# Performance work log

Hardware: AMD Instinct MI355X
Metric: run time of the kernel (lower is better)

Reference implementation:

```python
import jax, jax.numpy as jnp
import numpy as np

B, T, D = 2, 2048, 1024
H, G, K = 16, 4, 64          # num_heads, num_kv_heads, head_dim
R = H // G                   # GQA repeat factor
F = 4096                     # mlp_dim
EPS = 1e-6


def rms_norm(x, scale, eps=EPS):
    var = jnp.mean(x.astype(jnp.float32) ** 2, axis=-1, keepdims=True)
    normed = x * jax.lax.rsqrt(var + eps)
    return (scale * normed).astype(x.dtype)


def apply_rope(x_BTHK, sin_BTK, cos_BTK):
    half = x_BTHK.shape[-1] // 2
    x1, x2 = x_BTHK[..., :half], x_BTHK[..., half:]
    s = sin_BTK[:, :, None, :]
    c = cos_BTK[:, :, None, :]
    return jnp.concatenate([x1 * c - x2 * s, x2 * c + x1 * s], axis=-1).astype(x_BTHK.dtype)


def setup_inputs() -> dict:
    key = jax.random.key(0)
    ks = jax.random.split(key, 12)
    hidden_BTD = jax.random.normal(ks[0], (B, T, D), jnp.float32)
    # rope tables: realistic sin/cos of position*inv_freq
    inv_freq = 1.0 / (10000.0 ** (jnp.arange(K // 2, dtype=jnp.float32) / (K // 2)))
    ang = jnp.arange(T, dtype=jnp.float32)[:, None] * inv_freq[None, :]  # [T, K/2]
    sin_BTK = jnp.broadcast_to(jnp.sin(ang)[None], (B, T, K // 2))
    cos_BTK = jnp.broadcast_to(jnp.cos(ang)[None], (B, T, K // 2))
    mask = jnp.broadcast_to(jnp.tril(jnp.ones((T, T), bool))[None], (B, T, T))
    sc = 1.0 / np.sqrt(D)
    scf = 1.0 / np.sqrt(F)
    return {
        "hidden_BTD": hidden_BTD, "sin_BTK": sin_BTK, "cos_BTK": cos_BTK, "mask": mask,
        "ln1_scale": jnp.ones((D,), jnp.float32),
        "ln2_scale": jnp.ones((D,), jnp.float32),
        "qn_scale": jnp.ones((K,), jnp.float32),
        "kn_scale": jnp.ones((K,), jnp.float32),
        "q_w": jax.random.normal(ks[1], (D, H * K), jnp.float32) * sc,
        "k_w": jax.random.normal(ks[2], (D, G * K), jnp.float32) * sc,
        "v_w": jax.random.normal(ks[3], (D, G * K), jnp.float32) * sc,
        "o_w": jax.random.normal(ks[4], (H * K, D), jnp.float32) * sc,
        "gate_w": jax.random.normal(ks[5], (D, F), jnp.float32) * sc,
        "up_w": jax.random.normal(ks[6], (D, F), jnp.float32) * sc,
        "down_w": jax.random.normal(ks[7], (F, D), jnp.float32) * scf,
    }


def reference(hidden_BTD, sin_BTK, cos_BTK, mask, ln1_scale, ln2_scale,
              qn_scale, kn_scale, q_w, k_w, v_w, o_w, gate_w, up_w, down_w):
    x = rms_norm(hidden_BTD, ln1_scale)
    q = rms_norm((x @ q_w).reshape(B, T, H, K), qn_scale)
    k = rms_norm((x @ k_w).reshape(B, T, G, K), kn_scale)
    v = (x @ v_w).reshape(B, T, G, K)
    q = apply_rope(q, sin_BTK, cos_BTK)
    k = apply_rope(k, sin_BTK, cos_BTK)
    q_BTGRK = q.reshape(B, T, G, R, K)
    scale = K ** (-0.5)
    logits = jnp.einsum('BTGRK,BSGK->BTSGR', q_BTGRK, k) * scale
    neg = float(jnp.finfo(logits.dtype).min)
    logits = jnp.where(mask[:, :, :, None, None], logits, neg)
    weights = jax.nn.softmax(logits.astype(jnp.float32), axis=2).astype(logits.dtype)
    attn = jnp.einsum('BTSGR,BSGK->BTGRK', weights, v).reshape(B, T, H * K)
    hidden_BTD = hidden_BTD + attn @ o_w
    y = rms_norm(hidden_BTD, ln2_scale)
    ff = (jax.nn.silu(y @ gate_w) * (y @ up_w)) @ down_w
    return hidden_BTD + ff
```

## Files before the change

kernel.cpp:

```cpp
#include <hip/hip_runtime.h>
#include <hip/hip_bf16.h>

#define EPSF 1e-6f
constexpr int Bsz  = 2;
constexpr int Tseq = 2048;
constexpr int Dmod = 1024;
constexpr int Hh   = 16;
constexpr int Gg   = 4;
constexpr int Ff   = 4096;
constexpr int Mrows = Bsz * Tseq;

typedef __attribute__((ext_vector_type(8))) short bf16x8;
typedef __attribute__((ext_vector_type(4))) float f32x4;
typedef unsigned short u16;

__device__ inline u16 f2bf(float x) {
    union { float f; unsigned u; } v; v.f = x;
    unsigned r = v.u + 0x7fff + ((v.u >> 16) & 1);
    return (u16)(r >> 16);
}
__device__ inline float bf2f(u16 h) {
    union { unsigned u; float f; } v; v.u = ((unsigned)h) << 16; return v.f;
}

__device__ __forceinline__ void async_copy16(const u16* g, u16* l) {
    __builtin_amdgcn_global_load_lds(
        (const __attribute__((address_space(1))) void*)g,
        (__attribute__((address_space(3))) void*)l, 16, 0, 0);
}


__global__ __launch_bounds__(256) void wprep_all_kernel(
    const float* __restrict__ q_w, const float* __restrict__ k_w,
    const float* __restrict__ v_w, const float* __restrict__ o_w,
    const float* __restrict__ gate_w, const float* __restrict__ up_w,
    const float* __restrict__ down_w,
    u16* __restrict__ QKVT, u16* __restrict__ OTh, u16* __restrict__ OTl,
    u16* __restrict__ GTh, u16* __restrict__ UTh, u16* __restrict__ DTh)
{
    const int bx = blockIdx.x;
    const float* W; u16* Th; u16* Tl = nullptr;
    int N, Kd, ntile, ktile, drow;
    if (bx < 1024) {
        W = q_w; N = 1024; Kd = 1024; ntile = bx & 31; ktile = bx >> 5;
        Th = QKVT; drow = ntile * 32;
    } else if (bx < 1280) {
        const int i = bx - 1024;
        W = k_w; N = 256; Kd = 1024; ntile = i & 7; ktile = i >> 3;
        Th = QKVT; drow = 1024 + ntile * 32;
    } else if (bx < 1536) {
        const int i = bx - 1280;
        W = v_w; N = 256; Kd = 1024; ntile = i & 7; ktile = i >> 3;
        Th = QKVT; drow = 1280 + ntile * 32;
    } else if (bx < 2560) {
        const int i = bx - 1536;
        W = o_w; N = 1024; Kd = 1024; ntile = i & 31; ktile = i >> 5;
        Th = OTh; Tl = OTl; drow = ntile * 32;
    } else if (bx < 6656) {
        const int i = bx - 2560;
        W = gate_w; N = 4096; Kd = 1024; ntile = i & 127; ktile = i >> 7;
        Th = GTh; drow = ntile * 32;
    } else if (bx < 10752) {
        const int i = bx - 6656;
        W = up_w; N = 4096; Kd = 1024; ntile = i & 127; ktile = i >> 7;
        Th = UTh; drow = ntile * 32;
    } else {
        const int i = bx - 10752;
        W = down_w; N = 1024; Kd = 4096; ntile = i & 31; ktile = i >> 5;
        Th = DTh; drow = ntile * 32;
    }
    const int n0 = ntile * 32, k0 = ktile * 32;

    __shared__ float tile[32][33];
    const int r = threadIdx.x >> 3, c4 = (threadIdx.x & 7) * 4;
    const float4 v = *reinterpret_cast<const float4*>(&W[(size_t)(k0 + r) * N + n0 + c4]);
    tile[r][c4 + 0] = v.x; tile[r][c4 + 1] = v.y;
    tile[r][c4 + 2] = v.z; tile[r][c4 + 3] = v.w;
    __syncthreads();
    const int nl = threadIdx.x >> 3, kq = (threadIdx.x & 7) * 4;
    float x0 = tile[kq + 0][nl], x1 = tile[kq + 1][nl];
    float x2 = tile[kq + 2][nl], x3 = tile[kq + 3][nl];
    ushort4 h;
    h.x = f2bf(x0); h.y = f2bf(x1); h.z = f2bf(x2); h.w = f2bf(x3);
    *reinterpret_cast<ushort4*>(&Th[(size_t)(drow + nl) * Kd + k0 + kq]) = h;
    if (Tl) {
        ushort4 l;
        l.x = f2bf(x0 - bf2f(h.x)); l.y = f2bf(x1 - bf2f(h.y));
        l.z = f2bf(x2 - bf2f(h.z)); l.w = f2bf(x3 - bf2f(h.w));
        *reinterpret_cast<ushort4*>(&Tl[(size_t)(drow + nl) * Kd + k0 + kq]) = l;
    }
}

template <int LO>
__global__ __launch_bounds__(256) void rmsnorm_split_kernel(
    const float* __restrict__ x, const float* __restrict__ scale,
    u16* __restrict__ oh, u16* __restrict__ ol)
{
    const int row = blockIdx.x;
    const int tid = threadIdx.x;
    const float4 v = reinterpret_cast<const float4*>(x + (size_t)row * Dmod)[tid];
    float ss = v.x * v.x + v.y * v.y + v.z * v.z + v.w * v.w;
    #pragma unroll
    for (int off = 32; off; off >>= 1) ss += __shfl_xor(ss, off, 64);
    __shared__ float part[4];
    if ((tid & 63) == 0) part[tid >> 6] = ss;
    __syncthreads();
    const float tot = part[0] + part[1] + part[2] + part[3];
    const float rstd = rsqrtf(tot * (1.0f / Dmod) + EPSF);
    const float4 sc = reinterpret_cast<const float4*>(scale)[tid];
    float o0 = v.x * rstd * sc.x, o1 = v.y * rstd * sc.y;
    float o2 = v.z * rstd * sc.z, o3 = v.w * rstd * sc.w;
    ushort4 h;
    h.x = f2bf(o0); h.y = f2bf(o1); h.z = f2bf(o2); h.w = f2bf(o3);
    *reinterpret_cast<ushort4*>(&oh[(size_t)row * Dmod + tid * 4]) = h;
    if (LO) {
        ushort4 l;
        l.x = f2bf(o0 - bf2f(h.x)); l.y = f2bf(o1 - bf2f(h.y));
        l.z = f2bf(o2 - bf2f(h.z)); l.w = f2bf(o3 - bf2f(h.w));
        *reinterpret_cast<ushort4*>(&ol[(size_t)row * Dmod + tid * 4]) = l;
    }
}

template <int ASPLIT, int BSPLIT, int RES>
__global__ __launch_bounds__(256, 2) void mfma_gemm_kernel(
    const u16* __restrict__ Ah, const u16* __restrict__ Al,
    const u16* __restrict__ Bh, const u16* __restrict__ Bl,
    const float* __restrict__ res, float* __restrict__ C,
    int M, int N, int Kd)
{
    __shared__ u16 As_h[128 * 32];
    __shared__ u16 As_l[128 * 32];
    __shared__ u16 Bs_h[128 * 32];
    __shared__ u16 Bs_l[128 * 32];

    const int tid = threadIdx.x;
    const int lane = tid & 63, wave = tid >> 6;
    const int wm = (wave >> 1) * 64, wn = (wave & 1) * 64;
    const int m0 = blockIdx.y * 128, n0 = blockIdx.x * 128;
    const int fm = lane & 15, quad = lane >> 4;
    const int fsw = (fm >> 1) & 3;
    const int fcol = ((quad ^ fsw) * 8);

    f32x4 acc[4][4];
    #pragma unroll
    for (int i = 0; i < 4; ++i)
        #pragma unroll
        for (int j = 0; j < 4; ++j) acc[i][j] = (f32x4){0.f, 0.f, 0.f, 0.f};

    const int lrow = lane >> 2;
    const int lchunk = lane & 3;
    const int schunk = lchunk ^ ((lrow >> 1) & 3);

    for (int k0 = 0; k0 < Kd; k0 += 32) {
        __syncthreads();
        #pragma unroll
        for (int p = 0; p < 2; ++p) {
            const int row = wave * 32 + p * 16 + lrow;
            const size_t ga = (size_t)(m0 + row) * Kd + k0 + schunk * 8;
            const size_t gb = (size_t)(n0 + row) * Kd + k0 + schunk * 8;
            const int ls = row * 32 + lchunk * 8;
            async_copy16(&Ah[ga], &As_h[ls]);
            if (ASPLIT) async_copy16(&Al[ga], &As_l[ls]);
            async_copy16(&Bh[gb], &Bs_h[ls]);
            if (BSPLIT) async_copy16(&Bl[gb], &Bs_l[ls]);
        }
        __syncthreads();

        bf16x8 ah[4], al[4], bh[4], bl[4];
        #pragma unroll
        for (int t = 0; t < 4; ++t) {
            const int ra = (wm + t * 16 + fm) * 32 + fcol;
            const int rb = (wn + t * 16 + fm) * 32 + fcol;
            ah[t] = *reinterpret_cast<const bf16x8*>(&As_h[ra]);
            bh[t] = *reinterpret_cast<const bf16x8*>(&Bs_h[rb]);
            if (ASPLIT) al[t] = *reinterpret_cast<const bf16x8*>(&As_l[ra]);
            if (BSPLIT) bl[t] = *reinterpret_cast<const bf16x8*>(&Bs_l[rb]);
        }
        #pragma unroll
        for (int mt = 0; mt < 4; ++mt)
            #pragma unroll
            for (int nt = 0; nt < 4; ++nt) {
                acc[mt][nt] = __builtin_amdgcn_mfma_f32_16x16x32_bf16(
                    ah[mt], bh[nt], acc[mt][nt], 0, 0, 0);
                if (BSPLIT)
                    acc[mt][nt] = __builtin_amdgcn_mfma_f32_16x16x32_bf16(
                        ah[mt], bl[nt], acc[mt][nt], 0, 0, 0);
                if (ASPLIT)
                    acc[mt][nt] = __builtin_amdgcn_mfma_f32_16x16x32_bf16(
                        al[mt], bh[nt], acc[mt][nt], 0, 0, 0);
            }
    }

    const int cr = (lane >> 4) * 4, cn = lane & 15;
    #pragma unroll
    for (int mt = 0; mt < 4; ++mt)
        #pragma unroll
        for (int nt = 0; nt < 4; ++nt)
            #pragma unroll
            for (int r = 0; r < 4; ++r) {
                const int gm = m0 + wm + mt * 16 + cr + r;
                const int gn = n0 + wn + nt * 16 + cn;
                float v = acc[mt][nt][r];
                if (RES) v += res[(size_t)gm * N + gn];
                C[(size_t)gm * N + gn] = v;
            }
}

__global__ __launch_bounds__(256, 2) void qkv_fused_kernel(
    const u16* __restrict__ Ah, const u16* __restrict__ Bh,
    const float* __restrict__ qn, const float* __restrict__ kn,
    const float* __restrict__ sinp, const float* __restrict__ cosp,
    u16* __restrict__ Qbh, u16* __restrict__ Qbl,
    u16* __restrict__ Kbh, u16* __restrict__ Kbl,
    u16* __restrict__ Vth, u16* __restrict__ Vtl)
{
    __shared__ u16 As_h[128 * 32];
    __shared__ u16 Bs_h[128 * 32];

    const int Kd = 1024;
    const int tid = threadIdx.x;
    const int lane = tid & 63, wave = tid >> 6;
    const int wm = (wave >> 1) * 64, wn = (wave & 1) * 64;
    const int m0 = blockIdx.y * 128, n0 = blockIdx.x * 128;
    const int fm = lane & 15, quad = lane >> 4;
    const int fsw = (fm >> 1) & 3;
    const int fcol = ((quad ^ fsw) * 8);

    f32x4 acc[4][4];
    #pragma unroll
    for (int i = 0; i < 4; ++i)
        #pragma unroll
        for (int j = 0; j < 4; ++j) acc[i][j] = (f32x4){0.f, 0.f, 0.f, 0.f};

    const int lrow = lane >> 2;
    const int lchunk = lane & 3;
    const int schunk = lchunk ^ ((lrow >> 1) & 3);

    for (int k0 = 0; k0 < Kd; k0 += 32) {
        __syncthreads();
        #pragma unroll
        for (int p = 0; p < 2; ++p) {
            const int row = wave * 32 + p * 16 + lrow;
            const size_t ga = (size_t)(m0 + row) * Kd + k0 + schunk * 8;
            const size_t gb = (size_t)(n0 + row) * Kd + k0 + schunk * 8;
            const int ls = row * 32 + lchunk * 8;
            async_copy16(&Ah[ga], &As_h[ls]);
            async_copy16(&Bh[gb], &Bs_h[ls]);
        }
        __syncthreads();

        bf16x8 ah[4], bh[4];
        #pragma unroll
        for (int t = 0; t < 4; ++t) {
            ah[t] = *reinterpret_cast<const bf16x8*>(&As_h[(wm + t * 16 + fm) * 32 + fcol]);
            bh[t] = *reinterpret_cast<const bf16x8*>(&Bs_h[(wn + t * 16 + fm) * 32 + fcol]);
        }
        #pragma unroll
        for (int mt = 0; mt < 4; ++mt)
            #pragma unroll
            for (int nt = 0; nt < 4; ++nt)
                acc[mt][nt] = __builtin_amdgcn_mfma_f32_16x16x32_bf16(
                    ah[mt], bh[nt], acc[mt][nt], 0, 0, 0);
    }

    const int gn0 = n0 + wn;
    const int l15 = lane & 15;

    if (gn0 < 1280) {
        const bool isQ = (gn0 < 1024);
        const float* nsc = isQ ? qn : kn;
        const float osc = isQ ? 0.125f : 1.0f;
        u16* __restrict__ oh = isQ ? Qbh : Kbh;
        u16* __restrict__ ol = isQ ? Qbl : Kbl;
        const int rowstride = isQ ? 1024 : 256;
        const int colbase = isQ ? gn0 : gn0 - 1024;
        float sc[4];
        #pragma unroll
        for (int nt = 0; nt < 4; ++nt) sc[nt] = nsc[nt * 16 + l15];

        #pragma unroll
        for (int mt = 0; mt < 4; ++mt)
            #pragma unroll
            for (int r = 0; r < 4; ++r) {
                const int bt = m0 + wm + mt * 16 + quad * 4 + r;
                float v[4];
                #pragma unroll
                for (int nt = 0; nt < 4; ++nt) v[nt] = acc[mt][nt][r];
                float ss = v[0] * v[0] + v[1] * v[1] + v[2] * v[2] + v[3] * v[3];
                #pragma unroll
                for (int off = 1; off < 16; off <<= 1)
                    ss += __shfl_xor(ss, off, 16);
                const float rstd = rsqrtf(ss * (1.0f / 64.0f) + EPSF);
                float nv[4];
                #pragma unroll
                for (int nt = 0; nt < 4; ++nt) nv[nt] = v[nt] * rstd * sc[nt];
                const float s0 = sinp[bt * 32 + l15];
                const float c0 = cosp[bt * 32 + l15];
                const float s1 = sinp[bt * 32 + 16 + l15];
                const float c1 = cosp[bt * 32 + 16 + l15];
                float o[4];
                o[0] = (nv[0] * c0 - nv[2] * s0) * osc;
                o[1] = (nv[1] * c1 - nv[3] * s1) * osc;
                o[2] = (nv[2] * c0 + nv[0] * s0) * osc;
                o[3] = (nv[3] * c1 + nv[1] * s1) * osc;
                #pragma unroll
                for (int nt = 0; nt < 4; ++nt) {
                    const size_t off = (size_t)bt * rowstride + colbase + nt * 16 + l15;
                    const u16 hi = f2bf(o[nt]);
                    oh[off] = hi;
                    ol[off] = f2bf(o[nt] - bf2f(hi));
                }
            }
    } else {
        const int g = (gn0 - 1280) >> 6;
        const int b = (m0 + wm) >> 11;
        const int tb = ((m0 + wm) & 2047) + quad * 4;
        #pragma unroll
        for (int mt = 0; mt < 4; ++mt)
            #pragma unroll
            for (int nt = 0; nt < 4; ++nt) {
                const float v0 = acc[mt][nt][0], v1 = acc[mt][nt][1];
                const float v2 = acc[mt][nt][2], v3 = acc[mt][nt][3];
                ushort4 hv, lv;
                hv.x = f2bf(v0); hv.y = f2bf(v1); hv.z = f2bf(v2); hv.w = f2bf(v3);
                lv.x = f2bf(v0 - bf2f(hv.x)); lv.y = f2bf(v1 - bf2f(hv.y));
                lv.z = f2bf(v2 - bf2f(hv.z)); lv.w = f2bf(v3 - bf2f(hv.w));
                const size_t off =
                    ((size_t)((b * 4 + g) * 64 + nt * 16 + l15)) * Tseq + tb + mt * 16;
                *reinterpret_cast<ushort4*>(&Vth[off]) = hv;
                *reinterpret_cast<ushort4*>(&Vtl[off]) = lv;
            }
    }
}

__global__ __launch_bounds__(256, 2) void mfma_gateup_kernel(
    const u16* __restrict__ Ah, const u16* __restrict__ Al,
    const u16* __restrict__ Bg, const u16* __restrict__ Bu,
    u16* __restrict__ FF, int M, int N, int Kd)
{
    __shared__ u16 As_h[128 * 32];
    __shared__ u16 As_l[128 * 32];
    __shared__ u16 Gs[64 * 32];
    __shared__ u16 Us[64 * 32];

    const int tid = threadIdx.x;
    const int lane = tid & 63, wave = tid >> 6;
    const int wm = (wave >> 1) * 64, wn = (wave & 1) * 32;
    const int m0 = blockIdx.y * 128, n0 = blockIdx.x * 64;
    const int fm = lane & 15, quad = lane >> 4;
    const int fsw = (fm >> 1) & 3;
    const int fcol = ((quad ^ fsw) * 8);

    f32x4 accg[4][2], accu[4][2];
    #pragma unroll
    for (int i = 0; i < 4; ++i)
        #pragma unroll
        for (int j = 0; j < 2; ++j) {
            accg[i][j] = (f32x4){0.f, 0.f, 0.f, 0.f};
            accu[i][j] = (f32x4){0.f, 0.f, 0.f, 0.f};
        }

    const int lrow = lane >> 2;
    const int lchunk = lane & 3;
    const int schunk = lchunk ^ ((lrow >> 1) & 3);

    for (int k0 = 0; k0 < Kd; k0 += 32) {
        __syncthreads();
        #pragma unroll
        for (int p = 0; p < 2; ++p) {
            const int row = p * 64 + wave * 16 + lrow;
            const size_t ga = (size_t)(m0 + row) * Kd + k0 + schunk * 8;
            const int ls = row * 32 + lchunk * 8;
            async_copy16(&Ah[ga], &As_h[ls]);
            async_copy16(&Al[ga], &As_l[ls]);
        }
        {
            const int row = wave * 16 + lrow;
            const size_t gb = (size_t)(n0 + row) * Kd + k0 + schunk * 8;
            const int ls = row * 32 + lchunk * 8;
            async_copy16(&Bg[gb], &Gs[ls]);
            async_copy16(&Bu[gb], &Us[ls]);
        }
        __syncthreads();

        bf16x8 a_h[4], a_l[4], g_f[2], u_f[2];
        #pragma unroll
        for (int t = 0; t < 4; ++t) {
            const int ra = (wm + t * 16 + fm) * 32 + fcol;
            a_h[t] = *reinterpret_cast<const bf16x8*>(&As_h[ra]);
            a_l[t] = *reinterpret_cast<const bf16x8*>(&As_l[ra]);
        }
        #pragma unroll
        for (int j = 0; j < 2; ++j) {
            const int rb = (wn + j * 16 + fm) * 32 + fcol;
            g_f[j] = *reinterpret_cast<const bf16x8*>(&Gs[rb]);
            u_f[j] = *reinterpret_cast<const bf16x8*>(&Us[rb]);
        }
        #pragma unroll
        for (int mt = 0; mt < 4; ++mt)
            #pragma unroll
            for (int nt = 0; nt < 2; ++nt) {
                accg[mt][nt] = __builtin_amdgcn_mfma_f32_16x16x32_bf16(
                    a_h[mt], g_f[nt], accg[mt][nt], 0, 0, 0);
                accg[mt][nt] = __builtin_amdgcn_mfma_f32_16x16x32_bf16(
                    a_l[mt], g_f[nt], accg[mt][nt], 0, 0, 0);
                accu[mt][nt] = __builtin_amdgcn_mfma_f32_16x16x32_bf16(
                    a_h[mt], u_f[nt], accu[mt][nt], 0, 0, 0);
                accu[mt][nt] = __builtin_amdgcn_mfma_f32_16x16x32_bf16(
                    a_l[mt], u_f[nt], accu[mt][nt], 0, 0, 0);
            }
    }

    const int cr = (lane >> 4) * 4, cn = lane & 15;
    #pragma unroll
    for (int mt = 0; mt < 4; ++mt)
        #pragma unroll
        for (int nt = 0; nt < 2; ++nt)
            #pragma unroll
            for (int r = 0; r < 4; ++r) {
                const int gm = m0 + wm + mt * 16 + cr + r;
                const int gn = n0 + wn + nt * 16 + cn;
                const float g = accg[mt][nt][r];
                const float ff = (g / (1.0f + __expf(-g))) * accu[mt][nt][r];
                FF[(size_t)gm * N + gn] = f2bf(ff);
            }
}

__global__ __launch_bounds__(256) void attn_mfma_kernel(
    const u16* __restrict__ Qh, const u16* __restrict__ Ql,
    const u16* __restrict__ Kh, const u16* __restrict__ Kl,
    const u16* __restrict__ Vth, const u16* __restrict__ Vtl,
    u16* __restrict__ AOh, u16* __restrict__ AOl)
{
    __shared__ u16 KsH[64 * 72];
    __shared__ u16 KsL[64 * 72];
    __shared__ u16 VsH[64 * 72];
    __shared__ u16 VsL[64 * 72];
    __shared__ u16 Ps[4][16 * 72];

    const int tid = threadIdx.x;
    const int wave = tid >> 6, lane = tid & 63;
    const int l15 = lane & 15, quad = lane >> 4;

    const int bg = blockIdx.x & 7;
    const int b = bg >> 2, g = bg & 3;
    const int win = 127 - (blockIdx.x >> 3);
    const int t0 = win * 16;
    const int h = g * 4 + wave;

    bf16x8 qh[2], ql[2];
    {
        const size_t qrow = (size_t)(b * Tseq + t0 + l15) * 1024 + h * 64;
        #pragma unroll
        for (int ks = 0; ks < 2; ++ks) {
            qh[ks] = *reinterpret_cast<const bf16x8*>(&Qh[qrow + ks * 32 + quad * 8]);
            ql[ks] = *reinterpret_cast<const bf16x8*>(&Ql[qrow + ks * 32 + quad * 8]);
        }
    }

    const int srow = tid >> 2;
    const int scol = (tid & 3) * 16;
    const size_t kgb = (size_t)(b * Tseq) * 256 + g * 64 + scol;
    const size_t vgb = (size_t)(bg * 64 + srow) * Tseq + scol;

    const int nit = t0 / 64 + 1;

    uint4 ck0, ck1, cl0, cl1, cv0, cv1, cw0, cw1;
    {
        const size_t ka = kgb + (size_t)srow * 256;
        ck0 = *reinterpret_cast<const uint4*>(&Kh[ka]);
        ck1 = *reinterpret_cast<const uint4*>(&Kh[ka + 8]);
        cl0 = *reinterpret_cast<const uint4*>(&Kl[ka]);
        cl1 = *reinterpret_cast<const uint4*>(&Kl[ka + 8]);
        cv0 = *reinterpret_cast<const uint4*>(&Vth[vgb]);
        cv1 = *reinterpret_cast<const uint4*>(&Vth[vgb + 8]);
        cw0 = *reinterpret_cast<const uint4*>(&Vtl[vgb]);
        cw1 = *reinterpret_cast<const uint4*>(&Vtl[vgb + 8]);
    }

    f32x4 oacc[4];
    #pragma unroll
    for (int nt = 0; nt < 4; ++nt) oacc[nt] = (f32x4){0.f, 0.f, 0.f, 0.f};
    float m_r[4], l_r[4];
    #pragma unroll
    for (int r = 0; r < 4; ++r) { m_r[r] = -1e30f; l_r[r] = 0.0f; }

    u16* psw = &Ps[wave][0];
    const int lb = srow * 72 + scol;

    for (int it = 0; it < nit; ++it) {
        const int s0 = it * 64;
        const bool diag = (it == nit - 1);

        __syncthreads();
        *reinterpret_cast<uint4*>(&KsH[lb])     = ck0;
        *reinterpret_cast<uint4*>(&KsH[lb + 8]) = ck1;
        *reinterpret_cast<uint4*>(&KsL[lb])     = cl0;
        *reinterpret_cast<uint4*>(&KsL[lb + 8]) = cl1;
        *reinterpret_cast<uint4*>(&VsH[lb])     = cv0;
        *reinterpret_cast<uint4*>(&VsH[lb + 8]) = cv1;
        *reinterpret_cast<uint4*>(&VsL[lb])     = cw0;
        *reinterpret_cast<uint4*>(&VsL[lb + 8]) = cw1;
        if (it + 1 < nit) {
            const size_t ka = kgb + (size_t)(s0 + 64 + srow) * 256;
            ck0 = *reinterpret_cast<const uint4*>(&Kh[ka]);
            ck1 = *reinterpret_cast<const uint4*>(&Kh[ka + 8]);
            cl0 = *reinterpret_cast<const uint4*>(&Kl[ka]);
            cl1 = *reinterpret_cast<const uint4*>(&Kl[ka + 8]);
            const size_t va = vgb + s0 + 64;
            cv0 = *reinterpret_cast<const uint4*>(&Vth[va]);
            cv1 = *reinterpret_cast<const uint4*>(&Vth[va + 8]);
            cw0 = *reinterpret_cast<const uint4*>(&Vtl[va]);
            cw1 = *reinterpret_cast<const uint4*>(&Vtl[va + 8]);
        }
        __syncthreads();

        f32x4 sacc[4];
        #pragma unroll
        for (int nt = 0; nt < 4; ++nt) sacc[nt] = (f32x4){0.f, 0.f, 0.f, 0.f};

        #pragma unroll
        for (int ks = 0; ks < 2; ++ks) {
            bf16x8 kfh[4], kfl[4];
            #pragma unroll
            for (int nt = 0; nt < 4; ++nt) {
                const int a = (nt * 16 + l15) * 72 + ks * 32 + quad * 8;
                kfh[nt] = *reinterpret_cast<const bf16x8*>(&KsH[a]);
                kfl[nt] = *reinterpret_cast<const bf16x8*>(&KsL[a]);
            }
            #pragma unroll
            for (int nt = 0; nt < 4; ++nt) {
                sacc[nt] = __builtin_amdgcn_mfma_f32_16x16x32_bf16(qh[ks], kfh[nt], sacc[nt], 0, 0, 0);
                sacc[nt] = __builtin_amdgcn_mfma_f32_16x16x32_bf16(ql[ks], kfh[nt], sacc[nt], 0, 0, 0);
                sacc[nt] = __builtin_amdgcn_mfma_f32_16x16x32_bf16(qh[ks], kfl[nt], sacc[nt], 0, 0, 0);
            }
        }

        if (diag) {
            #pragma unroll
            for (int nt = 0; nt < 4; ++nt) {
                const int sg = s0 + nt * 16 + l15;
                #pragma unroll
                for (int r = 0; r < 4; ++r)
                    if (sg > t0 + quad * 4 + r) sacc[nt][r] = -1e30f;
            }
        }

        #pragma unroll
        for (int r = 0; r < 4; ++r) {
            float mx = fmaxf(fmaxf(sacc[0][r], sacc[1][r]),
                             fmaxf(sacc[2][r], sacc[3][r]));
            #pragma unroll
            for (int off = 1; off < 16; off <<= 1)
                mx = fmaxf(mx, __shfl_xor(mx, off, 16));
            const float mnew = fmaxf(m_r[r], mx);
            const float alpha = __expf(m_r[r] - mnew);
            m_r[r] = mnew;

            float rs = 0.0f;
            #pragma unroll
            for (int nt = 0; nt < 4; ++nt) {
                const float p = __expf(sacc[nt][r] - mnew);
                sacc[nt][r] = p;
                rs += p;
            }
            #pragma unroll
            for (int off = 1; off < 16; off <<= 1)
                rs += __shfl_xor(rs, off, 16);
            l_r[r] = l_r[r] * alpha + rs;
            #pragma unroll
            for (int nt = 0; nt < 4; ++nt) oacc[nt][r] *= alpha;
            #pragma unroll
            for (int nt = 0; nt < 4; ++nt)
                psw[(quad * 4 + r) * 72 + nt * 16 + l15] = f2bf(sacc[nt][r]);
        }

        #pragma unroll
        for (int ks = 0; ks < 2; ++ks) {
            const bf16x8 pa = *reinterpret_cast<const bf16x8*>(
                &psw[l15 * 72 + ks * 32 + quad * 8]);
            bf16x8 vfh[4], vfl[4];
            #pragma unroll
            for (int nt = 0; nt < 4; ++nt) {
                const int a = (nt * 16 + l15) * 72 + ks * 32 + quad * 8;
                vfh[nt] = *reinterpret_cast<const bf16x8*>(&VsH[a]);
                vfl[nt] = *reinterpret_cast<const bf16x8*>(&VsL[a]);
            }
            #pragma unroll
            for (int nt = 0; nt < 4; ++nt) {
                oacc[nt] = __builtin_amdgcn_mfma_f32_16x16x32_bf16(pa, vfh[nt], oacc[nt], 0, 0, 0);
                oacc[nt] = __builtin_amdgcn_mfma_f32_16x16x32_bf16(pa, vfl[nt], oacc[nt], 0, 0, 0);
            }
        }
    }

    #pragma unroll
    for (int r = 0; r < 4; ++r) {
        const float inv = 1.0f / l_r[r];
        const size_t orow = (size_t)(b * Tseq + t0 + quad * 4 + r) * 1024 + h * 64;
        #pragma unroll
        for (int nt = 0; nt < 4; ++nt) {
            const float o = oacc[nt][r] * inv;
            const u16 hi = f2bf(o);
            AOh[orow + nt * 16 + l15] = hi;
            AOl[orow + nt * 16 + l15] = f2bf(o - bf2f(hi));
        }
    }
}

extern "C" void kernel_launch(void* const* d_in, const int* in_sizes, int n_in,
                              void* d_out, int out_size, void* d_ws,
                              size_t ws_size, hipStream_t stream)
{
    const float* hidden = (const float*)d_in[0];
    const float* sinp   = (const float*)d_in[1];
    const float* cosp   = (const float*)d_in[2];
    const float* ln1    = (const float*)d_in[4];
    const float* ln2    = (const float*)d_in[5];
    const float* qn     = (const float*)d_in[6];
    const float* kn     = (const float*)d_in[7];
    const float* q_w    = (const float*)d_in[8];
    const float* k_w    = (const float*)d_in[9];
    const float* v_w    = (const float*)d_in[10];
    const float* o_w    = (const float*)d_in[11];
    const float* gate_w = (const float*)d_in[12];
    const float* up_w   = (const float*)d_in[13];
    const float* down_w = (const float*)d_in[14];
    float* out = (float*)d_out;

    char* base = (char*)d_ws;
    u16*   OTh  = (u16*)(base);
    u16*   OTl  = (u16*)(base + 2097152);
    u16*   GTh  = (u16*)(base + 4194304);
    u16*   UTh  = (u16*)(base + 12582912);
    u16*   DTh  = (u16*)(base + 20971520);
    u16*   QKVT = (u16*)(base + 29360128);
    u16*   Xh   = (u16*)(base + 32505856);
    u16*   Qbh  = (u16*)(base + 40894464);
    u16*   Qbl  = (u16*)(base + 49283072);
    u16*   Kbh  = (u16*)(base + 57671680);
    u16*   Kbl  = (u16*)(base + 59768832);
    u16*   Vth  = (u16*)(base + 61865984);
    u16*   Vtl  = (u16*)(base + 63963136);
    u16*   AOh  = (u16*)(base + 66060288);
    u16*   AOl  = (u16*)(base + 74448896);
    u16*   FFh  = (u16*)(base + 82837504);

    float* H2 = (float*)Qbh;
    u16*   Yh = Kbh;
    u16*   Yl = AOh;

    wprep_all_kernel<<<14848, 256, 0, stream>>>(
        q_w, k_w, v_w, o_w, gate_w, up_w, down_w,
        QKVT, OTh, OTl, GTh, UTh, DTh);

    rmsnorm_split_kernel<0><<<Mrows, 256, 0, stream>>>(hidden, ln1, Xh, nullptr);

    qkv_fused_kernel<<<dim3(12, 32), 256, 0, stream>>>(
        Xh, QKVT, qn, kn, sinp, cosp, Qbh, Qbl, Kbh, Kbl, Vth, Vtl);

    attn_mfma_kernel<<<Bsz * Gg * (Tseq / 16), 256, 0, stream>>>(
        Qbh, Qbl, Kbh, Kbl, Vth, Vtl, AOh, AOl);

    mfma_gemm_kernel<1, 1, 1><<<dim3(8, 32), 256, 0, stream>>>(
        AOh, AOl, OTh, OTl, hidden, H2, Mrows, Dmod, 1024);

    rmsnorm_split_kernel<1><<<Mrows, 256, 0, stream>>>(H2, ln2, Yh, Yl);

    mfma_gateup_kernel<<<dim3(Ff / 64, Mrows / 128), 256, 0, stream>>>(
        Yh, Yl, GTh, UTh, FFh, Mrows, Ff, 1024);

    mfma_gemm_kernel<0, 0, 1><<<dim3(8, 32), 256, 0, stream>>>(
        FFh, nullptr, DTh, nullptr, H2, out, Mrows, Dmod, 4096);
}
```

Before: 535.1 us.

## Rewrite gate/up GEMM with 256x128 tiles, triple-buffered async pipeline, XCD-aware mapping

Replaces the gate/up MLP GEMM with a 512-thread kernel that computes 256x128 output tiles per block. It triple-buffers A-high, A-low and weight tiles in LDS with async copies issued two k-steps ahead, and splits each k-step into four phases using barriers and MFMA priority hints. Block indices are remapped so that blocks on the same XCD share N tiles, for better L2 reuse. Each block now holds about 144KB of LDS, which conflicts with the two-blocks-per-CU launch bound and limits occupancy. The hand-placed waitcnt and barrier schedule is fragile.

New measurement: 521.5 us. 1.03x faster.

```diff
diff --git a/kernel.cpp b/kernel.cpp
--- a/kernel.cpp
+++ b/kernel.cpp
@@ -333,96 +333,179 @@
     }
 }
 
-__global__ __launch_bounds__(256, 2) void mfma_gateup_kernel(
-    const u16* __restrict__ Ah, const u16* __restrict__ Al,
-    const u16* __restrict__ Bg, const u16* __restrict__ Bu,
-    u16* __restrict__ FF, int M, int N, int Kd)
+#define GU_PHASE_SYNC()                                       \
+    __builtin_amdgcn_s_barrier();                             \
+    asm volatile("s_waitcnt lgkmcnt(0)" ::: "memory");        \
+    __builtin_amdgcn_sched_barrier(0)
+
+#define GU_MFMA4(MBASE, AF)                                                      \
+    _Pragma("unroll")                                                            \
+    for (int mf = 0; mf < 4; ++mf) {                                             \
+        accg[(MBASE) + mf][0] = __builtin_amdgcn_mfma_f32_16x16x32_bf16(         \
+            AF[mf], bgf[0], accg[(MBASE) + mf][0], 0, 0, 0);                     \
+        accu[(MBASE) + mf][0] = __builtin_amdgcn_mfma_f32_16x16x32_bf16(         \
+            AF[mf], buf2[0], accu[(MBASE) + mf][0], 0, 0, 0);                    \
+        accg[(MBASE) + mf][1] = __builtin_amdgcn_mfma_f32_16x16x32_bf16(         \
+            AF[mf], bgf[1], accg[(MBASE) + mf][1], 0, 0, 0);                     \
+        accu[(MBASE) + mf][1] = __builtin_amdgcn_mfma_f32_16x16x32_bf16(         \
+            AF[mf], buf2[1], accu[(MBASE) + mf][1], 0, 0, 0);                    \
+    }
+
+__global__ __launch_bounds__(512, 2) void gateup8_kernel(
+    const u16* __restrict__ Yh, const u16* __restrict__ Yl,
+    const u16* __restrict__ Gw, const u16* __restrict__ Uw,
+    u16* __restrict__ FF)
 {
-    __shared__ u16 As_h[128 * 32];
-    __shared__ u16 As_l[128 * 32];
-    __shared__ u16 Gs[64 * 32];
-    __shared__ u16 Us[64 * 32];
-
-    const int tid = threadIdx.x;
-    const int lane = tid & 63, wave = tid >> 6;
-    const int wm = (wave >> 1) * 64, wn = (wave & 1) * 32;
-    const int m0 = blockIdx.y * 128, n0 = blockIdx.x * 64;
+    constexpr int NK = 32;
+    __shared__ u16 AsH[3][256 * 32];
+    __shared__ u16 AsL[3][256 * 32];
+    __shared__ u16 Gs[3][128 * 32];
+    __shared__ u16 Us[3][128 * 32];
+
+    const int tid  = threadIdx.x;
+    const int lane = tid & 63;
+    const int wave = tid >> 6;
+    const int wave_m = wave >> 2;
+    const int wave_n = wave & 3;
+
+    const int wg  = blockIdx.x;
+    const int xcd = wg & 7;
+    const int idx = wg >> 3;
+    const int ntile = xcd * 4 + (idx & 3);
+    const int mtile = idx >> 2;
+    const int m0 = mtile * 256, n0 = ntile * 128;
+
     const int fm = lane & 15, quad = lane >> 4;
     const int fsw = (fm >> 1) & 3;
-    const int fcol = ((quad ^ fsw) * 8);
-
-    f32x4 accg[4][2], accu[4][2];
-    #pragma unroll
-    for (int i = 0; i < 4; ++i)
+    const int fcol = (quad ^ fsw) * 8;
+
+    f32x4 accg[8][2], accu[8][2];
+    #pragma unroll
+    for (int i = 0; i < 8; ++i)
         #pragma unroll
         for (int j = 0; j < 2; ++j) {
             accg[i][j] = (f32x4){0.f, 0.f, 0.f, 0.f};
             accu[i][j] = (f32x4){0.f, 0.f, 0.f, 0.f};
         }
 
-    const int lrow = lane >> 2;
-    const int lchunk = lane & 3;
-    const int schunk = lchunk ^ ((lrow >> 1) & 3);
-
-    for (int k0 = 0; k0 < Kd; k0 += 32) {
-        __syncthreads();
-        #pragma unroll
-        for (int p = 0; p < 2; ++p) {
-            const int row = p * 64 + wave * 16 + lrow;
-            const size_t ga = (size_t)(m0 + row) * Kd + k0 + schunk * 8;
-            const int ls = row * 32 + lchunk * 8;
-            async_copy16(&Ah[ga], &As_h[ls]);
-            async_copy16(&Al[ga], &As_l[ls]);
-        }
+    const int srow = tid >> 2;
+    const int schk = tid & 3;
+    const int sw   = schk ^ ((srow >> 1) & 3);
+    const u16* aSrc0 = &Yh[(size_t)(m0 + srow) * 1024 + sw * 8];
+    const u16* aSrc1 = &Yh[(size_t)(m0 + srow + 128) * 1024 + sw * 8];
+    const u16* lSrc0 = &Yl[(size_t)(m0 + srow) * 1024 + sw * 8];
+    const u16* lSrc1 = &Yl[(size_t)(m0 + srow + 128) * 1024 + sw * 8];
+    const u16* gSrc  = &Gw[(size_t)(n0 + srow) * 1024 + sw * 8];
+    const u16* uSrc  = &Uw[(size_t)(n0 + srow) * 1024 + sw * 8];
+    const int aDst0 = srow * 32 + schk * 8;
+    const int aDst1 = aDst0 + 128 * 32;
+
+#define STAGE_AH(T, BUF) do {                                  \
+        async_copy16(aSrc0 + (T) * 32, &AsH[BUF][aDst0]);      \
+        async_copy16(aSrc1 + (T) * 32, &AsH[BUF][aDst1]); } while (0)
+#define STAGE_AL(T, BUF) do {                                  \
+        async_copy16(lSrc0 + (T) * 32, &AsL[BUF][aDst0]);      \
+        async_copy16(lSrc1 + (T) * 32, &AsL[BUF][aDst1]); } while (0)
+#define STAGE_B(T, BUF) do {                                   \
+        async_copy16(gSrc + (T) * 32, &Gs[BUF][aDst0]);        \
+        async_copy16(uSrc + (T) * 32, &Us[BUF][aDst0]); } while (0)
+
+    int raOff[8], rbOff[2];
+    #pragma unroll
+    for (int mf = 0; mf < 8; ++mf)
+        raOff[mf] = (wave_m * 128 + mf * 16 + fm) * 32 + fcol;
+    #pragma unroll
+    for (int nf = 0; nf < 2; ++nf)
+        rbOff[nf] = (wave_n * 32 + nf * 16 + fm) * 32 + fcol;
+
+    STAGE_AH(0, 0); STAGE_AL(0, 0); STAGE_B(0, 0);
+    STAGE_AH(1, 1); STAGE_AL(1, 1); STAGE_B(1, 1);
+    asm volatile("s_waitcnt vmcnt(6)" ::: "memory");
+    __builtin_amdgcn_s_barrier();
+
+    int bcur = 0, bnxt = 2;
+    #pragma unroll 1
+    for (int t = 0; t < NK; ++t) {
+        const bool pf = (t + 2 < NK);
+        bf16x8 bgf[2], buf2[2];
+
         {
-            const int row = wave * 16 + lrow;
-            const size_t gb = (size_t)(n0 + row) * Kd + k0 + schunk * 8;
-            const int ls = row * 32 + lchunk * 8;
-            async_copy16(&Bg[gb], &Gs[ls]);
-            async_copy16(&Bu[gb], &Us[ls]);
-        }
-        __syncthreads();
-
-        bf16x8 a_h[4], a_l[4], g_f[2], u_f[2];
-        #pragma unroll
-        for (int t = 0; t < 4; ++t) {
-            const int ra = (wm + t * 16 + fm) * 32 + fcol;
-            a_h[t] = *reinterpret_cast<const bf16x8*>(&As_h[ra]);
-            a_l[t] = *reinterpret_cast<const bf16x8*>(&As_l[ra]);
-        }
-        #pragma unroll
-        for (int j = 0; j < 2; ++j) {
-            const int rb = (wn + j * 16 + fm) * 32 + fcol;
-            g_f[j] = *reinterpret_cast<const bf16x8*>(&Gs[rb]);
-            u_f[j] = *reinterpret_cast<const bf16x8*>(&Us[rb]);
-        }
-        #pragma unroll
-        for (int mt = 0; mt < 4; ++mt)
-            #pragma unroll
-            for (int nt = 0; nt < 2; ++nt) {
-                accg[mt][nt] = __builtin_amdgcn_mfma_f32_16x16x32_bf16(
-                    a_h[mt], g_f[nt], accg[mt][nt], 0, 0, 0);
-                accg[mt][nt] = __builtin_amdgcn_mfma_f32_16x16x32_bf16(
-                    a_l[mt], g_f[nt], accg[mt][nt], 0, 0, 0);
-                accu[mt][nt] = __builtin_amdgcn_mfma_f32_16x16x32_bf16(
-                    a_h[mt], u_f[nt], accu[mt][nt], 0, 0, 0);
-                accu[mt][nt] = __builtin_amdgcn_mfma_f32_16x16x32_bf16(
-                    a_l[mt], u_f[nt], accu[mt][nt], 0, 0, 0);
-            }
-    }
-
-    const int cr = (lane >> 4) * 4, cn = lane & 15;
-    #pragma unroll
-    for (int mt = 0; mt < 4; ++mt)
-        #pragma unroll
-        for (int nt = 0; nt < 2; ++nt)
+            #pragma unroll
+            for (int nf = 0; nf < 2; ++nf) {
+                bgf[nf]  = *reinterpret_cast<const bf16x8*>(&Gs[bcur][rbOff[nf]]);
+                buf2[nf] = *reinterpret_cast<const bf16x8*>(&Us[bcur][rbOff[nf]]);
+            }
+            bf16x8 af[4];
+            #pragma unroll
+            for (int mf = 0; mf < 4; ++mf)
+                af[mf] = *reinterpret_cast<const bf16x8*>(&AsH[bcur][raOff[mf]]);
+            if (pf) STAGE_AH(t + 2, bnxt);
+            GU_PHASE_SYNC();
+            __builtin_amdgcn_s_setprio(1);
+            GU_MFMA4(0, af);
+            __builtin_amdgcn_s_setprio(0);
+            __builtin_amdgcn_s_barrier();
+        }
+        {
+            bf16x8 af[4];
+            #pragma unroll
+            for (int mf = 0; mf < 4; ++mf)
+                af[mf] = *reinterpret_cast<const bf16x8*>(&AsH[bcur][raOff[mf + 4]]);
+            if (pf) STAGE_AL(t + 2, bnxt);
+            GU_PHASE_SYNC();
+            __builtin_amdgcn_s_setprio(1);
+            GU_MFMA4(4, af);
+            __builtin_amdgcn_s_setprio(0);
+            __builtin_amdgcn_s_barrier();
+        }
+        {
+            bf16x8 af[4];
+            #pragma unroll
+            for (int mf = 0; mf < 4; ++mf)
+                af[mf] = *reinterpret_cast<const bf16x8*>(&AsL[bcur][raOff[mf]]);
+            if (pf) STAGE_B(t + 2, bnxt);
+            GU_PHASE_SYNC();
+            __builtin_amdgcn_s_setprio(1);
+            GU_MFMA4(0, af);
+            __builtin_amdgcn_s_setprio(0);
+            __builtin_amdgcn_s_barrier();
+        }
+        {
+            bf16x8 af[4];
+            #pragma unroll
+            for (int mf = 0; mf < 4; ++mf)
+                af[mf] = *reinterpret_cast<const bf16x8*>(&AsL[bcur][raOff[mf + 4]]);
+            GU_PHASE_SYNC();
+            __builtin_amdgcn_s_setprio(1);
+            GU_MFMA4(4, af);
+            __builtin_amdgcn_s_setprio(0);
+            if (t + 2 < NK) {
+                asm volatile("s_waitcnt vmcnt(6)" ::: "memory");
+            } else if (t + 1 < NK) {
+                asm volatile("s_waitcnt vmcnt(0)" ::: "memory");
+            }
+            __builtin_amdgcn_s_barrier();
+        }
+
+        bcur = (bcur == 2) ? 0 : bcur + 1;
+        bnxt = (bnxt == 2) ? 0 : bnxt + 1;
+    }
+#undef STAGE_AH
+#undef STAGE_AL
+#undef STAGE_B
+
+    const int cr = quad * 4;
+    #pragma unroll
+    for (int mf = 0; mf < 8; ++mf)
+        #pragma unroll
+        for (int nf = 0; nf < 2; ++nf)
             #pragma unroll
             for (int r = 0; r < 4; ++r) {
-                const int gm = m0 + wm + mt * 16 + cr + r;
-                const int gn = n0 + wn + nt * 16 + cn;
-                const float g = accg[mt][nt][r];
-                const float ff = (g / (1.0f + __expf(-g))) * accu[mt][nt][r];
-                FF[(size_t)gm * N + gn] = f2bf(ff);
+                const int gm = m0 + wave_m * 128 + mf * 16 + cr + r;
+                const int gn = n0 + wave_n * 32 + nf * 16 + fm;
+                const float g = accg[mf][nf][r];
+                const float ff = (g / (1.0f + __expf(-g))) * accu[mf][nf][r];
+                FF[(size_t)gm * Ff + gn] = f2bf(ff);
             }
 }
 
@@ -667,8 +750,7 @@
 
     rmsnorm_split_kernel<1><<<Mrows, 256, 0, stream>>>(H2, ln2, Yh, Yl);
 
-    mfma_gateup_kernel<<<dim3(Ff / 64, Mrows / 128), 256, 0, stream>>>(
-        Yh, Yl, GTh, UTh, FFh, Mrows, Ff, 1024);
+    gateup8_kernel<<<512, 512, 0, stream>>>(Yh, Yl, GTh, UTh, FFh);
 
     mfma_gemm_kernel<0, 0, 1><<<dim3(8, 32), 256, 0, stream>>>(
         FFh, nullptr, DTh, nullptr, H2, out, Mrows, Dmod, 4096);
```
